# Kernel optimization log

Hardware: AMD Instinct MI355X
Metric: run time of the kernel (lower is better)

Reference implementation:

```python
import jax, jax.numpy as jnp
import numpy as np

B, TV, TS, D = 16, 256, 32, 512


def setup_inputs() -> dict:
    key = jax.random.key(0)
    ks = jax.random.split(key, 8)
    return {
        "video_feature": jax.random.normal(ks[0], (B, TV, D), dtype=jnp.float32),
        "video_mask": jnp.ones((B, TV), dtype=jnp.float32),
        "sentence_feature": jax.random.normal(ks[1], (B, TS, D), dtype=jnp.float32),
        "sentence_mask": jnp.ones((B, TS), dtype=jnp.float32),
        "w1": jax.random.normal(ks[2], (D, D), dtype=jnp.float32) * (1.0 / np.sqrt(D)),
        "b1": jax.random.normal(ks[3], (D,), dtype=jnp.float32) * 0.02,
        "w2": jax.random.normal(ks[4], (D, D), dtype=jnp.float32) * (1.0 / np.sqrt(D)),
        "wt": jax.random.normal(ks[5], (D,), dtype=jnp.float32) * (1.0 / np.sqrt(D)),
    }


def reference(video_feature, video_mask, sentence_feature, sentence_mask, w1, b1, w2, wt):
    # tmp1: [B, Tv, D] masked video projection (Linear with bias)
    tmp1 = (jnp.einsum("bvd,ed->bve", video_feature, w1) + b1) * video_mask[:, :, None]
    # tmp2: [B, Ts, D] masked sentence projection (Linear, no bias)
    tmp2 = jnp.einsum("bsd,ed->bse", sentence_feature, w2) * sentence_mask[:, :, None]
    # pairwise mask: [B, Tv, Ts]
    pair_mask = video_mask[:, :, None] * sentence_mask[:, None, :]
    # broadcast-add -> [B, Tv, Ts, D], mask, tanh, reduce with wt -> [B, Tv, Ts]
    tmp = (tmp1[:, :, None, :] + tmp2[:, None, :, :]) * pair_mask[..., None]
    M = jnp.einsum("bvsd,d->bvs", jnp.tanh(tmp), wt)
    return M * pair_mask
```

## Files before the change

kernel.cpp:

```cpp
#include <hip/hip_runtime.h>

#define BB 16
#define TV 256
#define TS 32
#define DD 512

typedef float    floatx4  __attribute__((ext_vector_type(4)));
typedef short    short8   __attribute__((ext_vector_type(8)));
typedef unsigned short ushort8 __attribute__((ext_vector_type(8)));

#define TANH_SCALE 2.885390082f

static __device__ __forceinline__ unsigned short f2bf(float f) {
    unsigned int u = __float_as_uint(f);
    u += 0x7FFFu + ((u >> 16) & 1u);
    return (unsigned short)(u >> 16);
}

__global__ __launch_bounds__(256) void ta_convert(
    const float* __restrict__ video, const float* __restrict__ sent,
    const float* __restrict__ w1,    const float* __restrict__ w2,
    unsigned short* __restrict__ vb, unsigned short* __restrict__ sb,
    unsigned short* __restrict__ w1b, unsigned short* __restrict__ w2b)
{
    const int NV = BB * TV * DD, NS = BB * TS * DD, NW = DD * DD;
    const int base = (blockIdx.x * 256 + threadIdx.x) * 8;
    const float* src; unsigned short* dst; int off;
    if      (base < NV)           { src = video; dst = vb;  off = base; }
    else if (base < NV + NS)      { src = sent;  dst = sb;  off = base - NV; }
    else if (base < NV + NS + NW) { src = w1;    dst = w1b; off = base - NV - NS; }
    else                          { src = w2;    dst = w2b; off = base - NV - NS - NW; }
    const float4 a = *(const float4*)(src + off);
    const float4 b = *(const float4*)(src + off + 4);
    ushort8 o;
    o[0] = f2bf(a.x); o[1] = f2bf(a.y); o[2] = f2bf(a.z); o[3] = f2bf(a.w);
    o[4] = f2bf(b.x); o[5] = f2bf(b.y); o[6] = f2bf(b.z); o[7] = f2bf(b.w);
    *(ushort8*)(dst + off) = o;
}

__global__ __launch_bounds__(256) void ta_mfma_gemm(
    const unsigned short* __restrict__ vb, const unsigned short* __restrict__ w1b,
    const float* __restrict__ b1,          const float* __restrict__ vmask,
    unsigned short* __restrict__ tmp1h,
    const unsigned short* __restrict__ sb, const unsigned short* __restrict__ w2b,
    const float* __restrict__ smask,       unsigned short* __restrict__ tmp2h,
    const float* __restrict__ wt,          float* __restrict__ wsum)
{
    const int t = threadIdx.x;

    if (blockIdx.x == 0 && t < 64) {
        float v = 0.f;
        for (int i = t; i < DD; i += 64) v += wt[i];
        for (int off = 32; off; off >>= 1) v += __shfl_down(v, off);
        if (t == 0) wsum[0] = v;
    }

    const bool g2 = (blockIdx.x >= 512);
    const int bid = g2 ? (int)blockIdx.x - 512 : (int)blockIdx.x;
    const unsigned short* __restrict__ A = g2 ? sb    : vb;
    const unsigned short* __restrict__ W = g2 ? w2b   : w1b;
    const float* __restrict__ rm         = g2 ? smask : vmask;
    const int m0 = (g2 ? (bid & 7)  : (bid & 63)) * 64;
    const int n0 = (g2 ? (bid >> 3) : (bid >> 6)) * 64;

    __shared__ unsigned short As[2][4096];
    __shared__ unsigned short Bs[2][4096];

    const int lane = t & 63;
    const int wid  = t >> 6;
    const int wm   = wid >> 1, wn = wid & 1;
    const int lr   = lane & 15, kg = lane >> 4;

    const int r0 = t >> 3,          g0c = (t & 7) ^ (r0 & 7);
    const int r1 = (t + 256) >> 3,  g1c = (t & 7) ^ (r1 & 7);
    const unsigned short* a0p = A + (size_t)(m0 + r0) * DD + g0c * 8;
    const unsigned short* a1p = A + (size_t)(m0 + r1) * DD + g1c * 8;
    const unsigned short* w0p = W + (size_t)(n0 + r0) * DD + g0c * 8;
    const unsigned short* w1p = W + (size_t)(n0 + r1) * DD + g1c * 8;
    const int l0 = t * 8;
    const int l1 = (t + 256) * 8;

#define TA_STAGE(buf, koff) do {                                               \
    __builtin_amdgcn_global_load_lds(                                          \
        (const __attribute__((address_space(1))) void*)(a0p + (koff)),         \
        (__attribute__((address_space(3))) void*)&As[buf][l0], 16, 0, 0);      \
    __builtin_amdgcn_global_load_lds(                                          \
        (const __attribute__((address_space(1))) void*)(a1p + (koff)),         \
        (__attribute__((address_space(3))) void*)&As[buf][l1], 16, 0, 0);      \
    __builtin_amdgcn_global_load_lds(                                          \
        (const __attribute__((address_space(1))) void*)(w0p + (koff)),         \
        (__attribute__((address_space(3))) void*)&Bs[buf][l0], 16, 0, 0);      \
    __builtin_amdgcn_global_load_lds(                                          \
        (const __attribute__((address_space(1))) void*)(w1p + (koff)),         \
        (__attribute__((address_space(3))) void*)&Bs[buf][l1], 16, 0, 0);      \
  } while (0)

    floatx4 acc[2][2] = {};

    const int ml0 = wm * 32 + lr, ml1 = ml0 + 16;
    const int nl0 = wn * 32 + lr, nl1 = nl0 + 16;
    const int sa0 = ml0 * 64, sa1 = ml1 * 64;
    const int sb0 = nl0 * 64, sb1 = nl1 * 64;
    const int xa = ml0 & 7, xb = nl0 & 7;

    TA_STAGE(0, 0);
    __syncthreads();

    int cur = 0;
    for (int step = 0; step < 8; ++step) {
        if (step < 7) TA_STAGE(cur ^ 1, (step + 1) * 64);
#pragma unroll
        for (int kk = 0; kk < 2; ++kk) {
            const int kc = kk * 4 + kg;
            short8 a0 = *(const short8*)&As[cur][sa0 + ((kc ^ xa) << 3)];
            short8 a1 = *(const short8*)&As[cur][sa1 + ((kc ^ xa) << 3)];
            short8 b0 = *(const short8*)&Bs[cur][sb0 + ((kc ^ xb) << 3)];
            short8 b1 = *(const short8*)&Bs[cur][sb1 + ((kc ^ xb) << 3)];
            acc[0][0] = __builtin_amdgcn_mfma_f32_16x16x32_bf16(a0, b0, acc[0][0], 0, 0, 0);
            acc[0][1] = __builtin_amdgcn_mfma_f32_16x16x32_bf16(a0, b1, acc[0][1], 0, 0, 0);
            acc[1][0] = __builtin_amdgcn_mfma_f32_16x16x32_bf16(a1, b0, acc[1][0], 0, 0, 0);
            acc[1][1] = __builtin_amdgcn_mfma_f32_16x16x32_bf16(a1, b1, acc[1][1], 0, 0, 0);
        }
        __syncthreads();
        cur ^= 1;
    }
#undef TA_STAGE

#pragma unroll
    for (int fm = 0; fm < 2; ++fm)
#pragma unroll
        for (int fn = 0; fn < 2; ++fn)
#pragma unroll
            for (int r = 0; r < 4; ++r) {
                const int m = m0 + wm * 32 + fm * 16 + kg * 4 + r;
                const int n = n0 + wn * 32 + fn * 16 + lr;
                const float mk = rm[m] * TANH_SCALE;
                float z = g2 ? (acc[fm][fn][r] * mk)
                             : (acc[fm][fn][r] + b1[n]) * mk;
                z = fminf(fmaxf(z, -30.f), 30.f);
                const float e = __builtin_amdgcn_exp2f(z);
                if (!g2) {
                    tmp1h[(size_t)m * DD + n] = f2bf(e);
                } else {
                    const int bb = m >> 5, ss = m & 31;
                    tmp2h[(size_t)bb * 16384 + (size_t)(ss >> 4) * 8192
                          + (size_t)(n >> 1) * 32 + (ss & 15) * 2 + (n & 1)] = f2bf(e);
                }
            }
}

__global__ __launch_bounds__(256) void ta_tanh_main(
    const unsigned short* __restrict__ tmp1h,
    const unsigned short* __restrict__ tmp2h,
    const float* __restrict__ wt,
    const float* __restrict__ wsum,
    const float* __restrict__ vmask,
    const float* __restrict__ smask,
    float* __restrict__ out)
{
    __shared__ unsigned int e2u[4096];
    __shared__ float part[512];

    const int t   = threadIdx.x;
    const int bid = blockIdx.x;
    const int b   = bid >> 7;
    const int vt  = (bid >> 1) & 63;
    const int sh  = bid & 1;
    const int v0  = vt << 2;

    {
        const ushort8* src = (const ushort8*)(tmp2h + (size_t)b * 16384 + sh * 8192);
        ushort8* dst = (ushort8*)e2u;
#pragma unroll
        for (int i = 0; i < 4; ++i) dst[t + 256 * i] = src[t + 256 * i];
    }
    __syncthreads();

    const int s  = t & 15;
    const int vi = (t >> 4) & 1;
    const int q  = t >> 5;

    const unsigned short* __restrict__ e1lo =
        tmp1h + (size_t)(b * TV + v0 + vi) * DD + q * 64;
    const unsigned short* __restrict__ e1hi = e1lo + 2 * DD;
    const float* __restrict__ wtp = wt + q * 64;
    const int ubase = (q * 32) * 16 + s;

    floatx4 alo = {0.f, 0.f, 0.f, 0.f};
    floatx4 ahi = {0.f, 0.f, 0.f, 0.f};
#pragma unroll 2
    for (int i = 0; i < 8; ++i) {
        const int ub = ubase + i * 64;
        const unsigned u0 = e2u[ub];
        const unsigned u1 = e2u[ub + 16];
        const unsigned u2 = e2u[ub + 32];
        const unsigned u3 = e2u[ub + 48];
        ushort8 l8 = *(const ushort8*)(e1lo + i * 8);
        ushort8 h8 = *(const ushort8*)(e1hi + i * 8);
        floatx4 wa = *(const floatx4*)(wtp + i * 8);
        floatx4 wb = *(const floatx4*)(wtp + i * 8 + 4);
        const float e2v[8] = {
            __uint_as_float(u0 << 16), __uint_as_float(u0 & 0xffff0000u),
            __uint_as_float(u1 << 16), __uint_as_float(u1 & 0xffff0000u),
            __uint_as_float(u2 << 16), __uint_as_float(u2 & 0xffff0000u),
            __uint_as_float(u3 << 16), __uint_as_float(u3 & 0xffff0000u)
        };
#pragma unroll
        for (int j = 0; j < 4; ++j) {
            const float xl = __uint_as_float((unsigned)l8[j] << 16);
            const float xh = __uint_as_float((unsigned)h8[j] << 16);
            const float dlo = fmaf(xl, e2v[j], 1.f);
            const float dhi = fmaf(xh, e2v[j], 1.f);
            const float inv = __builtin_amdgcn_rcpf(dlo * dhi);
            alo[j] = fmaf(wa[j], dhi * inv, alo[j]);
            ahi[j] = fmaf(wa[j], dlo * inv, ahi[j]);
        }
#pragma unroll
        for (int j = 0; j < 4; ++j) {
            const float xl = __uint_as_float((unsigned)l8[j + 4] << 16);
            const float xh = __uint_as_float((unsigned)h8[j + 4] << 16);
            const float dlo = fmaf(xl, e2v[j + 4], 1.f);
            const float dhi = fmaf(xh, e2v[j + 4], 1.f);
            const float inv = __builtin_amdgcn_rcpf(dlo * dhi);
            alo[j] = fmaf(wb[j], dhi * inv, alo[j]);
            ahi[j] = fmaf(wb[j], dlo * inv, ahi[j]);
        }
    }

    part[(vi    ) * 128 + s * 8 + q] = (alo[0] + alo[1]) + (alo[2] + alo[3]);
    part[(vi + 2) * 128 + s * 8 + q] = (ahi[0] + ahi[1]) + (ahi[2] + ahi[3]);
    __syncthreads();

    if (t < 64) {
        const int vrow = t >> 4, s2 = t & 15;
        const floatx4 p0 = *(const floatx4*)&part[vrow * 128 + s2 * 8];
        const floatx4 p1 = *(const floatx4*)&part[vrow * 128 + s2 * 8 + 4];
        const float sum = ((p0[0] + p0[1]) + (p0[2] + p0[3]))
                        + ((p1[0] + p1[1]) + (p1[2] + p1[3]));
        const int v  = v0 + vrow;
        const int sg = sh * 16 + s2;
        const float pm = vmask[b * TV + v] * smask[b * TS + sg];
        out[((size_t)b * TV + v) * TS + sg] = pm * (wsum[0] - 2.f * sum);
    }
}

extern "C" void kernel_launch(void* const* d_in, const int* in_sizes, int n_in,
                              void* d_out, int out_size, void* d_ws, size_t ws_size,
                              hipStream_t stream)
{
    const float* video = (const float*)d_in[0];
    const float* vmask = (const float*)d_in[1];
    const float* sent  = (const float*)d_in[2];
    const float* smask = (const float*)d_in[3];
    const float* w1    = (const float*)d_in[4];
    const float* b1    = (const float*)d_in[5];
    const float* w2    = (const float*)d_in[6];
    const float* wt    = (const float*)d_in[7];
    float* out = (float*)d_out;

    const size_t NV = (size_t)BB * TV * DD, NS = (size_t)BB * TS * DD, NW = (size_t)DD * DD;

    unsigned short* tmp1h = (unsigned short*)d_ws;
    unsigned short* tmp2h = tmp1h + NV;
    unsigned short* vb    = tmp2h + NS;
    unsigned short* sb    = vb + NV;
    unsigned short* w1b   = sb + NS;
    unsigned short* w2b   = w1b + NW;
    float* wsum           = (float*)(w2b + NW);

    const int total8 = (int)((NV + NS + 2 * NW) / 8);
    ta_convert<<<dim3(total8 / 256), dim3(256), 0, stream>>>(
        video, sent, w1, w2, vb, sb, w1b, w2b);
    ta_mfma_gemm<<<dim3(512 + 64), dim3(256), 0, stream>>>(
        vb, w1b, b1, vmask, tmp1h, sb, w2b, smask, tmp2h, wt, wsum);
    ta_tanh_main<<<dim3(BB * (TV / 4) * 2), dim3(256), 0, stream>>>(
        tmp1h, tmp2h, wt, wsum, vmask, smask, out);
}
```

Baseline: 35.76 us.

## Stage tmp1 rows in LDS via direct global-to-LDS loads, use two reciprocals

```diff
diff --git a/kernel.cpp b/kernel.cpp
--- a/kernel.cpp
+++ b/kernel.cpp
@@ -149,7 +149,7 @@
             }
 }
 
-__global__ __launch_bounds__(256) void ta_tanh_main(
+__global__ __launch_bounds__(256, 6) void ta_tanh_main(
     const unsigned short* __restrict__ tmp1h,
     const unsigned short* __restrict__ tmp2h,
     const float* __restrict__ wt,
@@ -158,7 +158,8 @@
     const float* __restrict__ smask,
     float* __restrict__ out)
 {
-    __shared__ unsigned int e2u[4096];
+    __shared__ unsigned int   e2u[4096];
+    __shared__ unsigned short e1u[4 * 520];
     __shared__ float part[512];
 
     const int t   = threadIdx.x;
@@ -169,10 +170,18 @@
     const int v0  = vt << 2;
 
     {
-        const ushort8* src = (const ushort8*)(tmp2h + (size_t)b * 16384 + sh * 8192);
-        ushort8* dst = (ushort8*)e2u;
-#pragma unroll
-        for (int i = 0; i < 4; ++i) dst[t + 256 * i] = src[t + 256 * i];
+        const unsigned short* e2src = tmp2h + (size_t)b * 16384 + sh * 8192 + t * 8;
+#pragma unroll
+        for (int i = 0; i < 4; ++i) {
+            __builtin_amdgcn_global_load_lds(
+                (const __attribute__((address_space(1))) void*)(e2src + i * 2048),
+                (__attribute__((address_space(3))) void*)&e2u[t * 4 + i * 1024], 16, 0, 0);
+        }
+        const int row = t >> 6, col = (t & 63) * 8;
+        __builtin_amdgcn_global_load_lds(
+            (const __attribute__((address_space(1))) void*)
+                (tmp1h + (size_t)(b * TV + v0 + row) * DD + col),
+            (__attribute__((address_space(3))) void*)&e1u[row * 520 + col], 16, 0, 0);
     }
     __syncthreads();
 
@@ -180,15 +189,14 @@
     const int vi = (t >> 4) & 1;
     const int q  = t >> 5;
 
-    const unsigned short* __restrict__ e1lo =
-        tmp1h + (size_t)(b * TV + v0 + vi) * DD + q * 64;
-    const unsigned short* __restrict__ e1hi = e1lo + 2 * DD;
+    const unsigned short* __restrict__ e1lo = e1u + vi * 520 + q * 64;
+    const unsigned short* __restrict__ e1hi = e1u + (vi + 2) * 520 + q * 64;
     const float* __restrict__ wtp = wt + q * 64;
-    const int ubase = (q * 32) * 16 + s;
+    const int ubase = q * 512 + s;
 
     floatx4 alo = {0.f, 0.f, 0.f, 0.f};
     floatx4 ahi = {0.f, 0.f, 0.f, 0.f};
-#pragma unroll 2
+#pragma unroll
     for (int i = 0; i < 8; ++i) {
         const int ub = ubase + i * 64;
         const unsigned u0 = e2u[ub];
@@ -209,21 +217,19 @@
         for (int j = 0; j < 4; ++j) {
             const float xl = __uint_as_float((unsigned)l8[j] << 16);
             const float xh = __uint_as_float((unsigned)h8[j] << 16);
-            const float dlo = fmaf(xl, e2v[j], 1.f);
-            const float dhi = fmaf(xh, e2v[j], 1.f);
-            const float inv = __builtin_amdgcn_rcpf(dlo * dhi);
-            alo[j] = fmaf(wa[j], dhi * inv, alo[j]);
-            ahi[j] = fmaf(wa[j], dlo * inv, ahi[j]);
+            const float rl = __builtin_amdgcn_rcpf(fmaf(xl, e2v[j], 1.f));
+            const float rh = __builtin_amdgcn_rcpf(fmaf(xh, e2v[j], 1.f));
+            alo[j] = fmaf(wa[j], rl, alo[j]);
+            ahi[j] = fmaf(wa[j], rh, ahi[j]);
         }
 #pragma unroll
         for (int j = 0; j < 4; ++j) {
             const float xl = __uint_as_float((unsigned)l8[j + 4] << 16);
             const float xh = __uint_as_float((unsigned)h8[j + 4] << 16);
-            const float dlo = fmaf(xl, e2v[j + 4], 1.f);
-            const float dhi = fmaf(xh, e2v[j + 4], 1.f);
-            const float inv = __builtin_amdgcn_rcpf(dlo * dhi);
-            alo[j] = fmaf(wb[j], dhi * inv, alo[j]);
-            ahi[j] = fmaf(wb[j], dlo * inv, ahi[j]);
+            const float rl = __builtin_amdgcn_rcpf(fmaf(xl, e2v[j + 4], 1.f));
+            const float rh = __builtin_amdgcn_rcpf(fmaf(xh, e2v[j + 4], 1.f));
+            alo[j] = fmaf(wb[j], rl, alo[j]);
+            ahi[j] = fmaf(wb[j], rh, ahi[j]);
         }
     }
 
```

Result: no change. 35.28 us (-1.3%).
